# Kernel optimization log

Hardware: AMD Instinct MI355X
Metric: run time of the kernel (lower is better)

## Reference

```python
import jax, jax.numpy as jnp
import numpy as np
from jax import lax

DN = ('NDHWC', 'DHWIO', 'NDHWC')
SHAPE = (33, 33, 33)
B = 2
N = 40000
C = 64


def setup_inputs() -> dict:
    key = jax.random.key(0)
    ks = jax.random.split(key, 24)
    D, H, W = SHAPE
    # unique active voxel coords (batch, z, y, x)
    rng = np.random.default_rng(0)
    idx = rng.choice(B * D * H * W, size=N, replace=False)
    b = idx // (D * H * W)
    r = idx % (D * H * W)
    coors = np.stack([b, r // (H * W), (r // W) % H, r % W], axis=1).astype(np.int32)

    def w(k, shape, scale=0.1):
        return jax.random.normal(k, shape, jnp.float32) * scale

    inp = {
        'features': jax.random.normal(ks[0], (N, 3), jnp.float32),
        'coors': jnp.asarray(coors),
        'batch_size': B,
        'w1': w(ks[1], (3, 3, 3, 3, C), 0.2), 'b1': w(ks[2], (C,), 0.05),
        'w2': w(ks[3], (3, 3, 3, C, C), 0.05), 'b2': w(ks[4], (C,), 0.05),
        'w3': w(ks[5], (3, 3, 3, C, C), 0.05), 'b3': w(ks[6], (C,), 0.05),
        'wt': w(ks[7], (3, 3, 3, C, C), 0.05), 'bt': w(ks[8], (C,), 0.05),
        'w5': w(ks[9], (3, 3, 3, C, C), 0.05), 'b5': w(ks[10], (C,), 0.05),
    }
    # folded eval-mode BatchNorm: y = x*s + h  (s = gamma/sqrt(var+eps), h = beta - mean*s)
    for i, (sk, hk) in enumerate(zip(ks[11:16], ks[16:21]), start=1):
        inp[f's{i}'] = 1.0 + 0.1 * jax.random.normal(sk, (C,), jnp.float32)
        inp[f'h{i}'] = 0.05 * jax.random.normal(hk, (C,), jnp.float32)
    return inp


def _forward(features, coors, batch_size,
             w1, b1, w2, b2, w3, b3, wt, bt, w5, b5,
             s1, h1, s2, h2, s3, h3, s4, h4, s5, h5):
    D, H, W = SHAPE
    bi, zi, yi, xi = coors[:, 0], coors[:, 1], coors[:, 2], coors[:, 3]
    # densify SparseConvTensor (zeros at inactive sites) + active mask
    x = jnp.zeros((batch_size, D, H, W, features.shape[-1]), features.dtype)
    x = x.at[bi, zi, yi, xi].set(features)
    m = jnp.zeros((batch_size, D, H, W, 1), jnp.float32).at[bi, zi, yi, xi].set(1.0)
    ones3 = jnp.ones((3, 3, 3, 1, 1), jnp.float32)

    conv = lambda a, k, pad: lax.conv_general_dilated(a, k, (1, 1, 1), pad, dimension_numbers=DN)
    # masked BN(eval) + ReLU: applied only on active sites, background stays exactly 0
    act = lambda y, mm, s, h: jnp.where(mm, jax.nn.relu(y * s + h), 0.0)

    # SparseConv3d(3,64,3): valid conv; output actives = 1-dilation of input actives
    x = conv(x, w1, 'VALID')
    m1 = conv(m, ones3, 'VALID') > 0  # [B,31,31,31,1]
    x = act(x + b1, m1, s1, h1)

    # two SubMConv3d(64,64,3) sharing indice_key: same active set, SAME padding
    x = act(conv(x, w2, 'SAME') + b2, m1, s2, h2)
    x = act(conv(x, w3, 'SAME') + b3, m1, s3, h3)

    # SparseConvTranspose3d(64,64,3,2): out = (D-1)*2+3; actives = transposed dilation
    x = lax.conv_transpose(x, wt, (2, 2, 2), 'VALID', dimension_numbers=DN)
    mT = lax.conv_transpose(m1.astype(jnp.float32), ones3, (2, 2, 2), 'VALID', dimension_numbers=DN) > 0
    x = act(x + bt, mT, s4, h4)

    # ToDense -> dense Conv3d(64,64,3) -> BN -> ReLU (dense: applied everywhere)
    x = conv(x, w5, 'VALID') + b5
    x = jax.nn.relu(x * s5 + h5)
    return jnp.transpose(x, (0, 4, 1, 2, 3))  # NCDHW like spconv ToDense output


def reference(features, coors, batch_size,
              w1, b1, w2, b2, w3, b3, wt, bt, w5, b5,
              s1, h1, s2, h2, s3, h3, s4, h4, s5, h5):
    return _forward(features, coors, batch_size,
                    w1, b1, w2, b2, w3, b3, wt, bt, w5, b5,
                    s1, h1, s2, h2, s3, h3, s4, h4, s5, h5)
```

## Files before the change

### kernel.cpp

```cpp
#include <hip/hip_runtime.h>
#include <cstdint>

constexpr int BB = 2, C = 64;
constexpr int D1 = 31;
constexpr int DP = 33;
constexpr int D4 = 63;
constexpr int D5 = 61;
constexpr int D5CUBE = D5*D5*D5;

constexpr int NV1 = BB*D1*D1*D1;
constexpr int NVP = BB*DP*DP*DP;
constexpr int NV4 = BB*D4*D4*D4;
constexpr int NV5 = BB*D5*D5*D5;

constexpr size_t alup(size_t x) { return (x + 255) & ~(size_t)255; }
constexpr size_t OB_X0  = 0;
constexpr size_t OB_M0  = alup(OB_X0  + (size_t)NVP*3*4);
constexpr size_t OB_M1P = alup(OB_M0  + (size_t)NVP*4);
constexpr size_t OB_X1  = alup(OB_M1P + (size_t)NVP*4);
constexpr size_t OB_X2  = alup(OB_X1  + (size_t)NVP*64*2);
constexpr size_t OB_X3  = alup(OB_X2  + (size_t)NVP*64*2);
constexpr size_t OB_MT  = alup(OB_X3  + (size_t)NVP*64*2);
constexpr size_t OB_X4  = alup(OB_MT  + (size_t)NV4*4);
constexpr size_t OB_WB2 = alup(OB_X4  + (size_t)NV4*64*2);
constexpr size_t OB_WB3 = alup(OB_WB2 + (size_t)27*64*64*2);
constexpr size_t OB_WBT = alup(OB_WB3 + (size_t)27*64*64*2);
constexpr size_t OB_WB5 = alup(OB_WBT + (size_t)27*64*64*2);

typedef __attribute__((ext_vector_type(8))) short short8;
typedef __attribute__((ext_vector_type(4))) float f32x4;

__device__ inline unsigned short f2bf(float f) {
  unsigned int u = __float_as_uint(f);
  u = (u + 0x7FFFu + ((u >> 16) & 1u)) >> 16;
  return (unsigned short)u;
}

template<int DD>
__device__ inline void decodev(int vox, int& b, int& z, int& y, int& x) {
  x = vox % DD; int r = vox / DD;
  y = r % DD;   r /= DD;
  z = r % DD;   b = r / DD;
}

__device__ inline int xcd_swz(int bid, int nb) {
  int q = nb >> 3, r = nb & 7;
  int xcd = bid & 7, idx = bid >> 3;
  return (xcd < r ? xcd*(q+1) : r*(q+1) + (xcd - r)*q) + idx;
}

__global__ void k_scatter(const float* __restrict__ feat, const int* __restrict__ coors,
                          int n, float* __restrict__ x0, float* __restrict__ m0) {
  int i = blockIdx.x*blockDim.x + threadIdx.x;
  if (i >= n) return;
  int b = coors[4*i+0], z = coors[4*i+1], y = coors[4*i+2], x = coors[4*i+3];
  int v = ((b*DP + z)*DP + y)*DP + x;
  x0[v*3+0] = feat[3*i+0];
  x0[v*3+1] = feat[3*i+1];
  x0[v*3+2] = feat[3*i+2];
  m0[v] = 1.0f;
}

__global__ void __launch_bounds__(256)
k_conv1(const float* __restrict__ x0, const float* __restrict__ m0,
        unsigned short* __restrict__ x1, float* __restrict__ m1p,
        const float* __restrict__ w1, const float* __restrict__ b1,
        const float* __restrict__ s1, const float* __restrict__ h1) {
  long long t = (long long)blockIdx.x*blockDim.x + threadIdx.x;
  if (t >= (long long)NV1*C) return;
  int co  = (int)(t & 63);
  int vox = (int)(t >> 6);
  int b, z, y, x; decodev<D1>(vox, b, z, y, x);
  float sum = 0.f, mm = 0.f;
  #pragma unroll
  for (int kz=0; kz<3; kz++)
  #pragma unroll
  for (int ky=0; ky<3; ky++)
  #pragma unroll
  for (int kx=0; kx<3; kx++) {
    int iv = ((b*DP + z+kz)*DP + y+ky)*DP + (x+kx);
    mm += m0[iv];
    const float* px = x0 + iv*3;
    const float* pw = w1 + ((kz*3+ky)*3+kx)*3*64 + co;
    sum += px[0]*pw[0] + px[1]*pw[64] + px[2]*pw[128];
  }
  bool m = mm > 0.f;
  float o = m ? fmaxf((sum + b1[co])*s1[co] + h1[co], 0.f) : 0.f;
  size_t pOff = (size_t)(((b*DP + z+1)*DP + y+1)*DP + (x+1));
  x1[pOff*C + co] = f2bf(o);
  if (co == 0) m1p[pOff] = m ? 1.f : 0.f;
}

__global__ void k_repack(const float* __restrict__ w, unsigned short* __restrict__ dst) {
  int i = blockIdx.x*256 + threadIdx.x;
  if (i >= 27*64*64) return;
  int co = i & 63, k = (i >> 6) & 63, t = i >> 12;
  int kk = k >> 5, q = (k >> 3) & 3, j = k & 7, cb = co >> 4, l = q*16 + (co & 15);
  dst[(size_t)((t*2+kk)*4+cb)*512 + l*8 + j] = f2bf(w[i]);
}

template<int NA, int DOUT, int DIN>
__global__ void __launch_bounds__(256)
k_conv_mfma(const unsigned short* __restrict__ inBF, const unsigned short* __restrict__ wB,
            unsigned short* __restrict__ outPtr, const float* __restrict__ m1p,
            const float* __restrict__ bias, const float* __restrict__ s,
            const float* __restrict__ h) {
  constexpr int NVOX = BB*DOUT*DOUT*DOUT;
  const int lane = threadIdx.x & 63;
  const int wid  = threadIdx.x >> 6;
  const int wave = xcd_swz(blockIdx.x, gridDim.x)*4 + wid;
  const int vb   = wave * (NA*16);

  int rowb[NA];
  #pragma unroll
  for (int a = 0; a < NA; a++) {
    int vox = vb + a*16 + (lane & 15);
    vox = vox < NVOX ? vox : NVOX-1;
    int b, z, y, x; decodev<DOUT>(vox, b, z, y, x);
    rowb[a] = (((b*DIN + z)*DIN + y)*DIN + x)*64;
  }
  const int koff = (lane >> 4) * 8;

  f32x4 acc[NA][4];
  #pragma unroll
  for (int a = 0; a < NA; a++)
    #pragma unroll
    for (int cb = 0; cb < 4; cb++)
      acc[a][cb] = f32x4{0.f, 0.f, 0.f, 0.f};

  #pragma unroll 1
  for (int t = 0; t < 27; ++t) {
    int kz = t / 9, rr = t - kz*9;
    int ky = rr / 3, kx = rr - ky*3;
    const int toff = ((kz*DIN + ky)*DIN + kx)*64;
    #pragma unroll
    for (int kk = 0; kk < 2; ++kk) {
      short8 A[NA];
      #pragma unroll
      for (int a = 0; a < NA; a++)
        A[a] = *reinterpret_cast<const short8*>(inBF + rowb[a] + toff + kk*32 + koff);
      short8 Bv[4];
      const unsigned short* wp = wB + (size_t)(t*2+kk)*2048 + lane*8;
      #pragma unroll
      for (int cb = 0; cb < 4; cb++)
        Bv[cb] = *reinterpret_cast<const short8*>(wp + cb*512);
      #pragma unroll
      for (int a = 0; a < NA; a++)
        #pragma unroll
        for (int cb = 0; cb < 4; cb++)
          acc[a][cb] = __builtin_amdgcn_mfma_f32_16x16x32_bf16(A[a], Bv[cb], acc[a][cb], 0, 0, 0);
    }
  }

  float bv[4], sv[4], hv[4];
  #pragma unroll
  for (int cb = 0; cb < 4; cb++) {
    int c = cb*16 + (lane & 15);
    bv[cb] = bias[c]; sv[cb] = s[c]; hv[cb] = h[c];
  }

  #pragma unroll
  for (int a = 0; a < NA; a++)
    #pragma unroll
    for (int r = 0; r < 4; r++) {
      int vox = vb + a*16 + (lane >> 4)*4 + r;
      if (vox >= NVOX) continue;
      int b, z, y, x; decodev<DOUT>(vox, b, z, y, x);
      size_t pOff = (size_t)(((b*DP + z+1)*DP + y+1)*DP + (x+1));
      bool m = m1p[pOff] > 0.f;
      #pragma unroll
      for (int cb = 0; cb < 4; cb++) {
        float o = m ? fmaxf((acc[a][cb][r] + bv[cb])*sv[cb] + hv[cb], 0.f) : 0.f;
        outPtr[pOff*64 + cb*16 + (lane & 15)] = f2bf(o);
      }
    }
}

__global__ void __launch_bounds__(256)
k_maskT(const float* __restrict__ m1p, float* __restrict__ mt) {
  int vox = blockIdx.x*256 + threadIdx.x;
  if (vox >= NV4) return;
  int b, zo, yo, xo; decodev<D4>(vox, b, zo, yo, xo);
  float mm = 0.f;
  for (int kz = 0; kz < 3; kz++) {
    if ((zo + kz) & 1) continue;
    int izp = ((zo + kz - 2) >> 1) + 1;
    for (int ky = 0; ky < 3; ky++) {
      if ((yo + ky) & 1) continue;
      int iyp = ((yo + ky - 2) >> 1) + 1;
      for (int kx = 0; kx < 3; kx++) {
        if ((xo + kx) & 1) continue;
        int ixp = ((xo + kx - 2) >> 1) + 1;
        mm += m1p[((b*DP + izp)*DP + iyp)*DP + ixp];
      }
    }
  }
  mt[vox] = mm;
}

__global__ void __launch_bounds__(256)
k_convT_mfma(const unsigned short* __restrict__ x3, const unsigned short* __restrict__ wB,
             unsigned short* __restrict__ x4, const float* __restrict__ mt,
             const float* __restrict__ bias, const float* __restrict__ s,
             const float* __restrict__ h) {
  const int lane = threadIdx.x & 63;
  const int wid  = threadIdx.x >> 6;
  const int w    = xcd_swz(blockIdx.x, gridDim.x)*4 + wid;
  if (w >= BB*D4*D4) return;
  const int b  = w / (D4*D4);
  const int rm = w % (D4*D4);
  const int zo = rm / D4;
  const int yo = rm % D4;
  const int ii = lane & 15;
  const int koff = (lane >> 4) * 8;

  f32x4 acc[4][4];
  #pragma unroll
  for (int a = 0; a < 4; a++)
    #pragma unroll
    for (int cb = 0; cb < 4; cb++)
      acc[a][cb] = f32x4{0.f, 0.f, 0.f, 0.f};

  #pragma unroll 1
  for (int kz = 0; kz < 3; kz++) {
    if ((zo + kz) & 1) continue;
    const int izp = ((zo + kz - 2) >> 1) + 1;
    #pragma unroll 1
    for (int ky = 0; ky < 3; ky++) {
      if ((yo + ky) & 1) continue;
      const int iyp = ((yo + ky - 2) >> 1) + 1;
      const size_t planeBase = ((size_t)((b*DP + izp)*DP + iyp))*DP*64;
      #pragma unroll
      for (int kx = 0; kx < 3; kx++) {
        const int apar  = kx & 1;
        const int xoffE = ((kx + apar - 2) >> 1) + 1;
        const int t = (kz*3 + ky)*3 + kx;
        #pragma unroll
        for (int kk = 0; kk < 2; ++kk) {
          short8 Bv[4];
          const unsigned short* wpk = wB + (size_t)(t*2+kk)*2048 + lane*8;
          #pragma unroll
          for (int cb = 0; cb < 4; cb++)
            Bv[cb] = *reinterpret_cast<const short8*>(wpk + cb*512);
          #pragma unroll
          for (int ablk = 0; ablk < 2; ablk++) {
            const int ixp = ablk*16 + ii + xoffE;
            short8 A = *reinterpret_cast<const short8*>(x3 + planeBase + (size_t)ixp*64 + kk*32 + koff);
            const int afr = apar*2 + ablk;
            #pragma unroll
            for (int cb = 0; cb < 4; cb++)
              acc[afr][cb] = __builtin_amdgcn_mfma_f32_16x16x32_bf16(A, Bv[cb], acc[afr][cb], 0, 0, 0);
          }
        }
      }
    }
  }

  float bv[4], sv[4], hv[4];
  #pragma unroll
  for (int cb = 0; cb < 4; cb++) {
    int c = cb*16 + (lane & 15);
    bv[cb] = bias[c]; sv[cb] = s[c]; hv[cb] = h[c];
  }
  const int rowBase = ((b*D4 + zo)*D4 + yo)*D4;
  #pragma unroll
  for (int a = 0; a < 4; a++) {
    const int ablk = a & 1, apar = a >> 1;
    #pragma unroll
    for (int r = 0; r < 4; r++) {
      const int row = (lane >> 4)*4 + r;
      const int xo  = 2*(ablk*16 + row) + apar;
      if (xo >= D4) continue;
      const int vox = rowBase + xo;
      const bool m = mt[vox] > 0.f;
      #pragma unroll
      for (int cb = 0; cb < 4; cb++) {
        float o = m ? fmaxf((acc[a][cb][r] + bv[cb])*sv[cb] + hv[cb], 0.f) : 0.f;
        x4[(size_t)vox*64 + cb*16 + (lane & 15)] = f2bf(o);
      }
    }
  }
}

constexpr int C5_CHUNKS = 3072;

__device__ __forceinline__ void c5_ldW(const unsigned short* __restrict__ wB, int wslot,
                                       int lane, short8 (&W)[4]) {
  const unsigned short* wp = wB + (size_t)wslot*2048 + lane*8;
  #pragma unroll
  for (int cb = 0; cb < 4; cb++)
    W[cb] = *reinterpret_cast<const short8*>(wp + cb*512);
}

__device__ __forceinline__ void c5_ldA(const short8* __restrict__ sb, int rb, int kx,
                                       int kkc, int l16, const int (&va)[4], short8 (&A)[4]) {
  #pragma unroll
  for (int a = 0; a < 4; a++) {
    int v  = va[a] + kx;
    int ch = ((rb + v) << 3) + ((kkc + l16) ^ (v & 7));
    A[a] = sb[ch];
  }
}

__device__ __forceinline__ void c5_step(const short8 (&A)[4], const short8 (&W)[4],
                                        f32x4 (&acc)[4][4]) {
  #pragma unroll
  for (int a = 0; a < 4; a++)
    #pragma unroll
    for (int cb = 0; cb < 4; cb++)
      acc[a][cb] = __builtin_amdgcn_mfma_f32_16x16x32_bf16(W[cb], A[a], acc[a][cb], 0, 0, 0);
}

__global__ void __launch_bounds__(256, 3)
k_conv5_mfma(const unsigned short* __restrict__ x4, const unsigned short* __restrict__ wB,
             float* __restrict__ out, const float* __restrict__ bias,
             const float* __restrict__ s, const float* __restrict__ h) {
  __shared__ short8 sbuf[C5_CHUNKS];
  const int tid  = threadIdx.x;
  const int lane = tid & 63;
  const int wid  = tid >> 6;
  const int ll   = lane & 15;
  const int l16  = lane >> 4;

  const int blk   = xcd_swz(blockIdx.x, gridDim.x);
  const int ytile = blk & 15;
  const int rzb   = blk >> 4;
  const int z     = rzb % D5;
  const int b     = rzb / D5;
  const int y0    = ytile * 4;

  int srcoff[12];
  #pragma unroll
  for (int it = 0; it < 12; ++it) {
    int g = it*256 + tid; if (g >= 3024) g -= 3024;
    int r = g / 504, rem = g - r*504;
    int v = rem >> 3, c16p = rem & 7;
    int c16l = c16p ^ (v & 7);
    int yin = y0 + r; yin = yin > D4-1 ? D4-1 : yin;
    srcoff[it] = ((yin*D4 + v) << 7) + (c16l << 4);
  }

  int va[4];
  #pragma unroll
  for (int a = 0; a < 4; a++) va[a] = a*16 + ll;

  f32x4 acc[4][4];
  #pragma unroll
  for (int a = 0; a < 4; a++)
    #pragma unroll
    for (int cb = 0; cb < 4; cb++)
      acc[a][cb] = f32x4{0.f, 0.f, 0.f, 0.f};

  const char* x4b = (const char*)x4;
  char* lbase = (char*)&sbuf[0];

  #pragma unroll 1
  for (int kz = 0; kz < 3; ++kz) {
    size_t pb = (size_t)(b*D4 + z + kz) * (D4*D4*128);
    #pragma unroll
    for (int it = 0; it < 12; ++it) {
      __builtin_amdgcn_global_load_lds(
        (const __attribute__((address_space(1))) void*)(x4b + pb + srcoff[it]),
        (__attribute__((address_space(3))) void*)(lbase + it*4096 + wid*1024),
        16, 0, 0);
    }
    short8 A0[4], W0[4], A1[4], W1[4];
    c5_ldW(wB, kz*18 + 0, lane, W0);
    __syncthreads();

    c5_ldA(sbuf, wid*63, 0, 0, l16, va, A0);
    #pragma unroll 1
    for (int ss = 0; ss < 18; ss += 2) {
      {
        int sn = ss + 1;
        int ky = sn/6, m6 = sn - ky*6, kx = m6 >> 1, kk = m6 & 1;
        c5_ldA(sbuf, (wid+ky)*63, kx, kk*4, l16, va, A1);
        c5_ldW(wB, kz*18 + sn, lane, W1);
      }
      c5_step(A0, W0, acc);
      if (ss + 2 < 18) {
        int sn = ss + 2;
        int ky = sn/6, m6 = sn - ky*6, kx = m6 >> 1, kk = m6 & 1;
        c5_ldA(sbuf, (wid+ky)*63, kx, kk*4, l16, va, A0);
        c5_ldW(wB, kz*18 + sn, lane, W0);
      } else if (kz < 2) {
        c5_ldW(wB, (kz+1)*18, lane, W0);
      }
      c5_step(A1, W1, acc);
    }
    __syncthreads();
  }

  const int yout = y0 + wid;
  if (yout < D5) {
    #pragma unroll
    for (int a = 0; a < 4; a++) {
      int x = va[a];
      if (x >= D5) continue;
      size_t sp = (size_t)(z*D5 + yout)*D5 + x;
      #pragma unroll
      for (int cb = 0; cb < 4; cb++)
        #pragma unroll
        for (int r = 0; r < 4; r++) {
          int co = cb*16 + l16*4 + r;
          float o = fmaxf((acc[a][cb][r] + bias[co])*s[co] + h[co], 0.f);
          out[(size_t)(b*64 + co)*D5CUBE + sp] = o;
        }
    }
  }
}

extern "C" void kernel_launch(void* const* d_in, const int* in_sizes, int n_in,
                              void* d_out, int out_size, void* d_ws, size_t ws_size,
                              hipStream_t stream) {
  const float* feat  = (const float*)d_in[0];
  const int*   coors = (const int*)d_in[1];
  const float* w1 = (const float*)d_in[3];
  const float* b1 = (const float*)d_in[4];
  const float* w2 = (const float*)d_in[5];
  const float* b2 = (const float*)d_in[6];
  const float* w3 = (const float*)d_in[7];
  const float* b3 = (const float*)d_in[8];
  const float* wt = (const float*)d_in[9];
  const float* bt = (const float*)d_in[10];
  const float* w5 = (const float*)d_in[11];
  const float* b5 = (const float*)d_in[12];
  const float* s1 = (const float*)d_in[13];
  const float* h1 = (const float*)d_in[14];
  const float* s2 = (const float*)d_in[15];
  const float* h2 = (const float*)d_in[16];
  const float* s3 = (const float*)d_in[17];
  const float* h3 = (const float*)d_in[18];
  const float* s4 = (const float*)d_in[19];
  const float* h4 = (const float*)d_in[20];
  const float* s5 = (const float*)d_in[21];
  const float* h5 = (const float*)d_in[22];
  int n = in_sizes[0] / 3;

  char* wsb = (char*)d_ws;
  float*          X0  = (float*)(wsb + OB_X0);
  float*          M0  = (float*)(wsb + OB_M0);
  float*          M1P = (float*)(wsb + OB_M1P);
  unsigned short* X1  = (unsigned short*)(wsb + OB_X1);
  unsigned short* X2  = (unsigned short*)(wsb + OB_X2);
  unsigned short* X3  = (unsigned short*)(wsb + OB_X3);
  float*          MT  = (float*)(wsb + OB_MT);
  unsigned short* X4  = (unsigned short*)(wsb + OB_X4);
  unsigned short* WB2 = (unsigned short*)(wsb + OB_WB2);
  unsigned short* WB3 = (unsigned short*)(wsb + OB_WB3);
  unsigned short* WBT = (unsigned short*)(wsb + OB_WBT);
  unsigned short* WB5 = (unsigned short*)(wsb + OB_WB5);

  hipMemsetAsync(wsb, 0, OB_MT, stream);

  k_repack<<<432, 256, 0, stream>>>(w2, WB2);
  k_repack<<<432, 256, 0, stream>>>(w3, WB3);
  k_repack<<<432, 256, 0, stream>>>(wt, WBT);
  k_repack<<<432, 256, 0, stream>>>(w5, WB5);

  k_scatter<<<(n+255)/256, 256, 0, stream>>>(feat, coors, n, X0, M0);

  {
    long long threads = (long long)NV1*C;
    k_conv1<<<(int)((threads+255)/256), 256, 0, stream>>>(X0, M0, X1, M1P, w1, b1, s1, h1);
  }

  constexpr int WAVES23 = (NV1 + 31) / 32;
  constexpr int BLK23   = (WAVES23 + 3) / 4;
  k_conv_mfma<2, D1, DP><<<BLK23, 256, 0, stream>>>(X1, WB2, X2, M1P, b2, s2, h2);
  k_conv_mfma<2, D1, DP><<<BLK23, 256, 0, stream>>>(X2, WB3, X3, M1P, b3, s3, h3);

  k_maskT<<<(NV4 + 255)/256, 256, 0, stream>>>(M1P, MT);

  constexpr int ROWS_T = BB*D4*D4;
  k_convT_mfma<<<(ROWS_T + 3)/4, 256, 0, stream>>>(X3, WBT, X4, MT, bt, s4, h4);

  constexpr int BLK5 = BB * D5 * 16;
  k_conv5_mfma<<<BLK5, 256, 0, stream>>>(X4, WB5, (float*)d_out, b5, s5, h5);
}
```

Measured before the change: 377.2 us.

## Double-buffer conv5 LDS staging per (kz,ky) and merge weight repack launches

The final dense conv kernel now stages one input y-plane slab per (kz,ky) into two alternating LDS buffers. The next slab is prefetched with global_load_lds while the MFMAs run on the current one, replacing the old single buffer that held the whole kz slab and forced a sync between stages. LDS use rises from 48KB to 64KB and the occupancy hint drops from 3 to 2 blocks, trading occupancy for overlap. Separately, the four weight repack launches are merged into one kernel to cut launch overhead.

```diff
diff --git a/kernel.cpp b/kernel.cpp
--- a/kernel.cpp
+++ b/kernel.cpp
@@ -91,9 +91,14 @@
   if (co == 0) m1p[pOff] = m ? 1.f : 0.f;
 }
 
-__global__ void k_repack(const float* __restrict__ w, unsigned short* __restrict__ dst) {
-  int i = blockIdx.x*256 + threadIdx.x;
-  if (i >= 27*64*64) return;
+__global__ void k_repack4(const float* __restrict__ wa, const float* __restrict__ wb,
+                          const float* __restrict__ wc, const float* __restrict__ wd,
+                          unsigned short* __restrict__ da, unsigned short* __restrict__ db,
+                          unsigned short* __restrict__ dc, unsigned short* __restrict__ dd) {
+  int which = blockIdx.x / 432;
+  int i = (blockIdx.x - which*432)*256 + threadIdx.x;
+  const float* w = which == 0 ? wa : which == 1 ? wb : which == 2 ? wc : wd;
+  unsigned short* dst = which == 0 ? da : which == 1 ? db : which == 2 ? dc : dd;
   int co = i & 63, k = (i >> 6) & 63, t = i >> 12;
   int kk = k >> 5, q = (k >> 3) & 3, j = k & 7, cb = co >> 4, l = q*16 + (co & 15);
   dst[(size_t)((t*2+kk)*4+cb)*512 + l*8 + j] = f2bf(w[i]);
@@ -282,26 +287,6 @@
   }
 }
 
-constexpr int C5_CHUNKS = 3072;
-
-__device__ __forceinline__ void c5_ldW(const unsigned short* __restrict__ wB, int wslot,
-                                       int lane, short8 (&W)[4]) {
-  const unsigned short* wp = wB + (size_t)wslot*2048 + lane*8;
-  #pragma unroll
-  for (int cb = 0; cb < 4; cb++)
-    W[cb] = *reinterpret_cast<const short8*>(wp + cb*512);
-}
-
-__device__ __forceinline__ void c5_ldA(const short8* __restrict__ sb, int rb, int kx,
-                                       int kkc, int l16, const int (&va)[4], short8 (&A)[4]) {
-  #pragma unroll
-  for (int a = 0; a < 4; a++) {
-    int v  = va[a] + kx;
-    int ch = ((rb + v) << 3) + ((kkc + l16) ^ (v & 7));
-    A[a] = sb[ch];
-  }
-}
-
 __device__ __forceinline__ void c5_step(const short8 (&A)[4], const short8 (&W)[4],
                                         f32x4 (&acc)[4][4]) {
   #pragma unroll
@@ -311,11 +296,11 @@
       acc[a][cb] = __builtin_amdgcn_mfma_f32_16x16x32_bf16(W[cb], A[a], acc[a][cb], 0, 0, 0);
 }
 
-__global__ void __launch_bounds__(256, 3)
+__global__ void __launch_bounds__(256, 2)
 k_conv5_mfma(const unsigned short* __restrict__ x4, const unsigned short* __restrict__ wB,
              float* __restrict__ out, const float* __restrict__ bias,
              const float* __restrict__ s, const float* __restrict__ h) {
-  __shared__ short8 sbuf[C5_CHUNKS];
+  __shared__ short8 sbuf[2][2048];
   const int tid  = threadIdx.x;
   const int lane = tid & 63;
   const int wid  = tid >> 6;
@@ -329,20 +314,18 @@
   const int b     = rzb / D5;
   const int y0    = ytile * 4;
 
-  int srcoff[12];
-  #pragma unroll
-  for (int it = 0; it < 12; ++it) {
-    int g = it*256 + tid; if (g >= 3024) g -= 3024;
+  int st_r[8], st_base[8];
+  #pragma unroll
+  for (int it = 0; it < 8; ++it) {
+    int g = it*256 + tid; g = g > 2015 ? 2015 : g;
     int r = g / 504, rem = g - r*504;
     int v = rem >> 3, c16p = rem & 7;
     int c16l = c16p ^ (v & 7);
-    int yin = y0 + r; yin = yin > D4-1 ? D4-1 : yin;
-    srcoff[it] = ((yin*D4 + v) << 7) + (c16l << 4);
-  }
-
-  int va[4];
-  #pragma unroll
-  for (int a = 0; a < 4; a++) va[a] = a*16 + ll;
+    st_r[it] = r;
+    st_base[it] = (v << 7) + (c16l << 4);
+  }
+
+  const char* x4b = (const char*)x4;
 
   f32x4 acc[4][4];
   #pragma unroll
@@ -351,42 +334,59 @@
     for (int cb = 0; cb < 4; cb++)
       acc[a][cb] = f32x4{0.f, 0.f, 0.f, 0.f};
 
-  const char* x4b = (const char*)x4;
-  char* lbase = (char*)&sbuf[0];
-
+  auto STAGE = [&](int kzn, int kyn, int hn) {
+    size_t pb = (size_t)(b*D4 + z + kzn) * (D4*D4*128);
+    char* dst = (char*)&sbuf[hn][0];
+    #pragma unroll
+    for (int it = 0; it < 8; ++it) {
+      int yin = y0 + st_r[it] + kyn; yin = yin > 62 ? 62 : yin;
+      __builtin_amdgcn_global_load_lds(
+        (const __attribute__((address_space(1))) void*)(x4b + pb + (size_t)yin*8064 + st_base[it]),
+        (__attribute__((address_space(3))) void*)(dst + it*4096 + wid*1024),
+        16, 0, 0);
+    }
+  };
+  auto LDA = [&](int hh, int kx, int kk, short8 (&A)[4]) {
+    #pragma unroll
+    for (int a = 0; a < 4; a++) {
+      int v  = a*16 + ll + kx;
+      int ch = wid*504 + v*8 + ((kk*4 + l16) ^ (v & 7));
+      A[a] = sbuf[hh][ch];
+    }
+  };
+  auto LDW = [&](int slot, short8 (&W)[4]) {
+    const unsigned short* wp = wB + (size_t)slot*2048 + lane*8;
+    #pragma unroll
+    for (int cb = 0; cb < 4; cb++)
+      W[cb] = *reinterpret_cast<const short8*>(wp + cb*512);
+  };
+
+  short8 A0[4], A1[4], W0[4], W1[4];
+
+  STAGE(0, 0, 0);
+  LDW(0, W0);
+  __syncthreads();
+
+  int kzn = 0, kyn = 1;
   #pragma unroll 1
-  for (int kz = 0; kz < 3; ++kz) {
-    size_t pb = (size_t)(b*D4 + z + kz) * (D4*D4*128);
-    #pragma unroll
-    for (int it = 0; it < 12; ++it) {
-      __builtin_amdgcn_global_load_lds(
-        (const __attribute__((address_space(1))) void*)(x4b + pb + srcoff[it]),
-        (__attribute__((address_space(3))) void*)(lbase + it*4096 + wid*1024),
-        16, 0, 0);
-    }
-    short8 A0[4], W0[4], A1[4], W1[4];
-    c5_ldW(wB, kz*18 + 0, lane, W0);
-    __syncthreads();
-
-    c5_ldA(sbuf, wid*63, 0, 0, l16, va, A0);
-    #pragma unroll 1
-    for (int ss = 0; ss < 18; ss += 2) {
-      {
-        int sn = ss + 1;
-        int ky = sn/6, m6 = sn - ky*6, kx = m6 >> 1, kk = m6 & 1;
-        c5_ldA(sbuf, (wid+ky)*63, kx, kk*4, l16, va, A1);
-        c5_ldW(wB, kz*18 + sn, lane, W1);
-      }
-      c5_step(A0, W0, acc);
-      if (ss + 2 < 18) {
-        int sn = ss + 2;
-        int ky = sn/6, m6 = sn - ky*6, kx = m6 >> 1, kk = m6 & 1;
-        c5_ldA(sbuf, (wid+ky)*63, kx, kk*4, l16, va, A0);
-        c5_ldW(wB, kz*18 + sn, lane, W0);
-      } else if (kz < 2) {
-        c5_ldW(wB, (kz+1)*18, lane, W0);
-      }
-      c5_step(A1, W1, acc);
+  for (int p = 0; p < 9; ++p) {
+    const int hh = p & 1;
+    if (p < 8) {
+      STAGE(kzn, kyn, hh ^ 1);
+      kyn++; if (kyn == 3) { kyn = 0; kzn++; }
+    }
+    LDA(hh, 0, 0, A0);
+    const int sbase = p*6;
+    #pragma unroll
+    for (int st = 0; st < 6; ++st) {
+      const int kxn = (st+1) >> 1, kkn = (st+1) & 1;
+      if (st < 5) {
+        if (st & 1) LDA(hh, kxn, kkn, A0); else LDA(hh, kxn, kkn, A1);
+      }
+      if (sbase + st + 1 < 54) {
+        if (st & 1) LDW(sbase + st + 1, W0); else LDW(sbase + st + 1, W1);
+      }
+      if (st & 1) c5_step(A1, W1, acc); else c5_step(A0, W0, acc);
     }
     __syncthreads();
   }
@@ -395,7 +395,7 @@
   if (yout < D5) {
     #pragma unroll
     for (int a = 0; a < 4; a++) {
-      int x = va[a];
+      int x = a*16 + ll;
       if (x >= D5) continue;
       size_t sp = (size_t)(z*D5 + yout)*D5 + x;
       #pragma unroll
@@ -453,10 +453,7 @@
 
   hipMemsetAsync(wsb, 0, OB_MT, stream);
 
-  k_repack<<<432, 256, 0, stream>>>(w2, WB2);
-  k_repack<<<432, 256, 0, stream>>>(w3, WB3);
-  k_repack<<<432, 256, 0, stream>>>(wt, WBT);
-  k_repack<<<432, 256, 0, stream>>>(w5, WB5);
+  k_repack4<<<1728, 256, 0, stream>>>(w2, w3, wt, w5, WB2, WB3, WBT, WB5);
 
   k_scatter<<<(n+255)/256, 256, 0, stream>>>(feat, coors, n, X0, M0);
 
```

New measurement: 372.2 us. No clear change (-1.3%).
